# Performance work log

Hardware: AMD Instinct MI355X
Metric: run time of the kernel (lower is better)

Reference implementation:

```python
import jax, jax.numpy as jnp
import numpy as np

N_USERS = 100000
N_ITEMS = 100000
D = 64
B = 2048


def _ancf_layer(q, keys, aW, ab, W1, W2):
    # AttentionMechanism: hidden = relu(keys @ aW.T + ab)  [N, d]
    hidden = jax.nn.relu(keys @ aW.T + ab)
    # scores [B, N]; softmax over keys (dim=1)
    attn = jax.nn.softmax(q @ hidden.T, axis=1)
    q2 = q + attn @ keys  # [B, d]
    # MessageAggregation loop collapsed algebraically:
    # out = W1(q2) + sum_j W1(k_j) + sum_j W2(q2 * k_j)
    #     = W1(q2) + W1(S) + W2(q2 * S),  S = sum_j k_j
    S = keys.sum(axis=0)  # [d]
    out = (q2 + S) @ W1.T + (q2 * S) @ W2.T
    return jax.nn.leaky_relu(out, 0.01)


def setup_inputs() -> dict:
    key = jax.random.key(0)
    ks = jax.random.split(key, 12)
    scale_emb = 0.1
    scale_w = (2.0 / (D + D)) ** 0.5  # xavier-normal std for square layers
    inp = {
        "user_emb": jax.random.normal(ks[0], (N_USERS, D), jnp.float32) * scale_emb,
        "item_emb": jax.random.normal(ks[1], (N_ITEMS, D), jnp.float32) * scale_emb,
        "u_attn_W": jax.random.normal(ks[2], (D, D), jnp.float32) * scale_w,
        "u_attn_b": jnp.zeros((D,), jnp.float32),
        "u_W1": jax.random.normal(ks[3], (D, D), jnp.float32) * scale_w,
        "u_W2": jax.random.normal(ks[4], (D, D), jnp.float32) * scale_w,
        "i_attn_W": jax.random.normal(ks[5], (D, D), jnp.float32) * scale_w,
        "i_attn_b": jnp.zeros((D,), jnp.float32),
        "i_W1": jax.random.normal(ks[6], (D, D), jnp.float32) * scale_w,
        "i_W2": jax.random.normal(ks[7], (D, D), jnp.float32) * scale_w,
        "user_id": jax.random.randint(ks[8], (B,), 0, N_USERS),
        "item_id": jax.random.randint(ks[9], (B,), 0, N_ITEMS),
        "all_user_ids": jnp.arange(N_USERS),
        "all_item_ids": jnp.arange(N_ITEMS),
    }
    return inp


def reference(user_emb, item_emb, u_attn_W, u_attn_b, u_W1, u_W2,
              i_attn_W, i_attn_b, i_W1, i_W2,
              user_id, item_id, all_user_ids, all_item_ids):
    all_user_embeddings = user_emb[all_user_ids]  # [N_users, d]
    all_item_embeddings = item_emb[all_item_ids]  # [N_items, d]
    ue = all_user_embeddings[user_id]  # [B, d]
    ie = all_item_embeddings[item_id]  # [B, d]

    ue_out = _ancf_layer(ue, all_item_embeddings, u_attn_W, u_attn_b, u_W1, u_W2)
    ie_out = _ancf_layer(ie, all_user_embeddings, i_attn_W, i_attn_b, i_W1, i_W2)

    og_user = jnp.concatenate([ue, ue_out], axis=1)  # [B, 2d]
    og_item = jnp.concatenate([ie, ie_out], axis=1)  # [B, 2d]
    return og_user.T @ og_item  # [2d, 2d]
```

## Files before the change

### kernel.cpp

```cpp
#include <hip/hip_runtime.h>


typedef __bf16 bf16x8 __attribute__((ext_vector_type(8)));
typedef float f32x2 __attribute__((ext_vector_type(2)));
typedef float f32x4 __attribute__((ext_vector_type(4)));
typedef float f32x16 __attribute__((ext_vector_type(16)));
typedef unsigned int u32x4 __attribute__((ext_vector_type(4)));
typedef int i32x4 __attribute__((ext_vector_type(4)));
typedef int i32x8 __attribute__((ext_vector_type(8)));

static constexpr int NKEYS  = 100000;
static constexpr int NP     = 102400;
static constexpr int DIM    = 64;
static constexpr int BQ     = 2048;
static constexpr int NCH    = 64;
static constexpr int CHROWS = NP / NCH;
static constexpr int NPH    = CHROWS / 64;
static constexpr int NTIL   = NP / 64;
static constexpr float PADCNT = float(NP - NKEYS);
static constexpr float LOG2E  = 1.44269504088896340736f;

#define DEVINL __device__ __forceinline__

DEVINL unsigned int cvtpk(float lo, float hi) {
    unsigned int r;
    asm("v_cvt_pk_bf16_f32 %0, %1, %2" : "=v"(r) : "v"(lo), "v"(hi));
    return r;
}
DEVINL unsigned short bfr(float f) {
    return (unsigned short)(cvtpk(f, f) & 0xffffu);
}
DEVINL float bf2f(unsigned short u) {
    unsigned int w = (unsigned int)u << 16;
    return __builtin_bit_cast(float, w);
}
DEVINL void permswap(unsigned int& a, unsigned int& b) {
    asm("v_permlane32_swap_b32 %0, %1" : "+v"(a), "+v"(b));
}
DEVINL bf16x8 pack_frag(unsigned int w0, unsigned int w1, unsigned int w2, unsigned int w3) {
    u32x4 t; t[0] = w0; t[1] = w1; t[2] = w2; t[3] = w3;
    return __builtin_bit_cast(bf16x8, t);
}
DEVINL bf16x8 frag8_f32(const float* p) {
    f32x4 a = *reinterpret_cast<const f32x4*>(p);
    f32x4 b = *reinterpret_cast<const f32x4*>(p + 4);
    return pack_frag(cvtpk(a[0], a[1]), cvtpk(a[2], a[3]),
                     cvtpk(b[0], b[1]), cvtpk(b[2], b[3]));
}
DEVINL unsigned int fp8x4(float a, float b, float c, float d) {
    int r = __builtin_amdgcn_cvt_pk_fp8_f32(a, b, 0, false);
    r = __builtin_amdgcn_cvt_pk_fp8_f32(c, d, r, true);
    return (unsigned int)r;
}
DEVINL unsigned char fp8b(float f) {
    return (unsigned char)(__builtin_amdgcn_cvt_pk_fp8_f32(f, f, 0, false) & 0xFF);
}
DEVINL i32x8 cat8(i32x4 a, i32x4 b) {
    return __builtin_shufflevector(a, b, 0, 1, 2, 3, 4, 5, 6, 7);
}
DEVINL f32x16 mfma8(i32x8 a, i32x8 b, f32x16 c) {
    return __builtin_amdgcn_mfma_scale_f32_32x32x64_f8f6f4(
        a, b, c, 0 , 0 ,
        0, 0x7F7F7F7F, 0, 0x7F7F7F7F);
}
DEVINL float fexp2(float x) {
    float f = __builtin_fmaf(x, 8388608.0f, 1065713994.0f);
    int i = (int)f;
    return __builtin_bit_cast(float, i);
}
DEVINL f32x2 pkadd(f32x2 a, f32x2 b) {
    f32x2 r;
    asm("v_pk_add_f32 %0, %1, %2" : "=v"(r) : "v"(a), "v"(b));
    return r;
}

__global__ __launch_bounds__(256) void prep_kernel(
    const float* __restrict__ user_emb, const float* __restrict__ item_emb,
    const float* __restrict__ uaW, const float* __restrict__ uab,
    const float* __restrict__ iaW, const float* __restrict__ iab,
    unsigned char* __restrict__ Khid, unsigned char* __restrict__ Vpan,
    float* __restrict__ csum)
{
    const int side = blockIdx.y;
    const int tile = blockIdx.x;
    const float* keys = (side == 0) ? item_emb : user_emb;
    const float* aW   = (side == 0) ? uaW : iaW;
    const float* ab   = (side == 0) ? uab : iab;
    unsigned char* Kh  = Khid + (size_t)side * NP * DIM;
    unsigned char* Vps = Vpan + (size_t)side * (NP / 32) * 2048;

    __shared__ float Kf[64][68];
    __shared__ float Wf[64][68];
    __shared__ float bl[64];

    const int t  = threadIdx.x;
    const int r  = t >> 2;
    const int c0 = (t & 3) * 16;

    {
        const float4* src = reinterpret_cast<const float4*>(aW + r * 64 + c0);
        float4* dst = reinterpret_cast<float4*>(&Wf[r][c0]);
        #pragma unroll
        for (int q = 0; q < 4; ++q) dst[q] = src[q];
        if (t < 64) bl[t] = ab[t];
    }
    {
        const int n = tile * 64 + r;
        float4* dst = reinterpret_cast<float4*>(&Kf[r][c0]);
        if (n < NKEYS) {
            const float4* src = reinterpret_cast<const float4*>(keys + (size_t)n * 64 + c0);
            #pragma unroll
            for (int q = 0; q < 4; ++q) dst[q] = src[q];
        } else {
            const float4 z = make_float4(0.f, 0.f, 0.f, 0.f);
            #pragma unroll
            for (int q = 0; q < 4; ++q) dst[q] = z;
        }
    }
    __syncthreads();

    {
        const int wv = t >> 6, lane = t & 63;
        const int c = lane & 31, hi = lane >> 5;
        const int n0 = (wv & 1) * 32, j0 = (wv >> 1) * 32;
        f32x16 acc{};
        #pragma unroll
        for (int ks = 0; ks < 4; ++ks) {
            bf16x8 af = frag8_f32(&Kf[n0 + c][ks * 16 + hi * 8]);
            bf16x8 bf_ = frag8_f32(&Wf[j0 + c][ks * 16 + hi * 8]);
            acc = __builtin_amdgcn_mfma_f32_32x32x16_bf16(af, bf_, acc, 0, 0, 0);
        }
        const float bj = bl[j0 + c];
        #pragma unroll
        for (int rr = 0; rr < 16; ++rr) {
            const int n  = n0 + (rr & 3) + 8 * (rr >> 2) + 4 * hi;
            const int gn = tile * 64 + n;
            float h = fmaxf(acc[rr] + bj, 0.f);
            if (gn >= NKEYS) h = 0.f;
            Kh[(size_t)gn * 64 + j0 + c] = fp8b(h);
        }
    }
    {
        unsigned int pw[4];
        #pragma unroll
        for (int j = 0; j < 4; ++j)
            pw[j] = fp8x4(Kf[c0 + 4 * j][r],     Kf[c0 + 4 * j + 1][r],
                          Kf[c0 + 4 * j + 2][r], Kf[c0 + 4 * j + 3][r]);
        unsigned char* dst = Vps + ((size_t)(2 * tile + (c0 >> 5))) * 2048 + r * 32 + (c0 & 31);
        *reinterpret_cast<uint4*>(dst) = make_uint4(pw[0], pw[1], pw[2], pw[3]);
    }
    if (t < 64) {
        float s = 0.f;
        #pragma unroll 8
        for (int rr = 0; rr < 64; ++rr) s += Kf[rr][t];
        csum[((size_t)side * NTIL + tile) * 64 + t] = s;
    }
}

__global__ __launch_bounds__(64) void sreduceA_kernel(const float* __restrict__ csum,
                                                      float* __restrict__ csum2)
{
    const int j = blockIdx.x, side = blockIdx.y, d = threadIdx.x;
    float s = 0.f;
    for (int idx = j; idx < NTIL; idx += 64)
        s += csum[((size_t)side * NTIL + idx) * 64 + d];
    csum2[((size_t)side * 64 + j) * 64 + d] = s;
}

__global__ __launch_bounds__(64) void sreduceB_kernel(const float* __restrict__ csum2,
                                                      float* __restrict__ Sbuf)
{
    const int side = blockIdx.x, d = threadIdx.x;
    float s = 0.f;
    #pragma unroll 8
    for (int j = 0; j < 64; ++j) s += csum2[((size_t)side * 64 + j) * 64 + d];
    Sbuf[side * 64 + d] = s;
}

__global__ __launch_bounds__(512) void flash_kernel(
    const float* __restrict__ user_emb, const float* __restrict__ item_emb,
    const int* __restrict__ user_id, const int* __restrict__ item_id,
    const unsigned char* __restrict__ Khid, const unsigned char* __restrict__ Vpan,
    unsigned short* __restrict__ Opart, float* __restrict__ lpart)
{
    const int side  = blockIdx.z;
    const int chunk = blockIdx.x;
    const int qblk  = blockIdx.y;
    const int wave  = threadIdx.x >> 6;
    const int lane  = threadIdx.x & 63;
    const int c  = lane & 31;
    const int hi = lane >> 5;

    __shared__ __align__(16) unsigned char KV[2][8192];

    const float* emb = (side == 0) ? user_emb : item_emb;
    const int* ids   = (side == 0) ? user_id  : item_id;
    const unsigned char* Kh = Khid + ((size_t)side * NP + (size_t)chunk * CHROWS) * 64;
    const unsigned char* Vb = Vpan + ((size_t)side * (NP / 32) + (size_t)chunk * (CHROWS / 32)) * 2048;

    const unsigned char* gsrc;
    if (wave < 4) {
        const int st = wave >> 1, qh = wave & 1;
        gsrc = Kh + st * 2048 + qh * 16 + c * 64 + hi * 32;
    } else {
        const int dblk = (wave - 4) >> 1, qh = wave & 1;
        gsrc = Vb + dblk * 1024 + qh * 16 + hi * 2048 + c * 32;
    }

    const unsigned char* gnext = gsrc;
    int ibuf = 0;
    auto ISSUE = [&]() {
        __builtin_amdgcn_global_load_lds(
            (const __attribute__((address_space(1))) unsigned int*)gnext,
            (__attribute__((address_space(3))) unsigned int*)&KV[ibuf][wave * 1024],
            16, 0, 0);
        gnext += 4096;
        ibuf ^= 1;
    };

    const int qtile = qblk * 256 + wave * 32;
    const int id = ids[qtile + c];
    const float* qrow = emb + (size_t)id * 64 + hi * 32;
    float4 qf[8];
    #pragma unroll
    for (int w = 0; w < 8; ++w)
        qf[w] = *reinterpret_cast<const float4*>(qrow + w * 4);

    ISSUE();

    i32x8 bq;
    #pragma unroll
    for (int w = 0; w < 8; ++w)
        bq[w] = (int)fp8x4(qf[w].x * LOG2E, qf[w].y * LOG2E,
                           qf[w].z * LOG2E, qf[w].w * LOG2E);

    f32x16 o0{}, o1{};
    f32x2 lacc[8] = {};

    asm volatile("s_waitcnt vmcnt(0)" ::: "memory");
    __builtin_amdgcn_s_barrier();

    for (int p = 0; p < NPH; ++p) {
        if (p + 1 < NPH) ISSUE();

        const unsigned char* Bp = &KV[p & 1][0];
        const int fo = hi * 512 + c * 16;

        i32x8 ak0 = cat8(*reinterpret_cast<const i32x4*>(Bp + fo),
                         *reinterpret_cast<const i32x4*>(Bp + 1024 + fo));
        i32x8 ak1 = cat8(*reinterpret_cast<const i32x4*>(Bp + 2048 + fo),
                         *reinterpret_cast<const i32x4*>(Bp + 3072 + fo));

        __builtin_amdgcn_s_setprio(1);
        f32x16 z{};
        f32x16 s0 = mfma8(ak0, bq, z);
        f32x16 s1 = mfma8(ak1, bq, z);
        __builtin_amdgcn_s_setprio(0);

        i32x8 bv0 = cat8(*reinterpret_cast<const i32x4*>(Bp + 4096 + fo),
                         *reinterpret_cast<const i32x4*>(Bp + 5120 + fo));
        i32x8 bv1 = cat8(*reinterpret_cast<const i32x4*>(Bp + 6144 + fo),
                         *reinterpret_cast<const i32x4*>(Bp + 7168 + fo));

        #pragma unroll
        for (int rr = 0; rr < 16; ++rr) s0[rr] = fexp2(s0[rr]);
        #pragma unroll
        for (int rr = 0; rr < 16; ++rr) s1[rr] = fexp2(s1[rr]);

        #pragma unroll
        for (int g = 0; g < 8; ++g) {
            f32x2 a; a[0] = s0[2 * g]; a[1] = s0[2 * g + 1];
            f32x2 b; b[0] = s1[2 * g]; b[1] = s1[2 * g + 1];
            lacc[g] = pkadd(lacc[g], pkadd(a, b));
        }

        unsigned int p0[4], p1[4];
        #pragma unroll
        for (int g = 0; g < 4; ++g) {
            p0[g] = fp8x4(s0[4 * g], s0[4 * g + 1], s0[4 * g + 2], s0[4 * g + 3]);
            p1[g] = fp8x4(s1[4 * g], s1[4 * g + 1], s1[4 * g + 2], s1[4 * g + 3]);
            permswap(p0[g], p1[g]);
        }
        i32x8 pa;
        pa[0] = (int)p0[0]; pa[1] = (int)p1[0];
        pa[2] = (int)p0[1]; pa[3] = (int)p1[1];
        pa[4] = (int)p0[2]; pa[5] = (int)p1[2];
        pa[6] = (int)p0[3]; pa[7] = (int)p1[3];

        __builtin_amdgcn_s_setprio(1);
        o0 = mfma8(pa, bv0, o0);
        o1 = mfma8(pa, bv1, o1);
        __builtin_amdgcn_s_setprio(0);

        if (p + 1 < NPH) {
            asm volatile("s_waitcnt vmcnt(0)" ::: "memory");
            __builtin_amdgcn_s_barrier();
        }
    }

    float ls = 0.f;
    #pragma unroll
    for (int g = 0; g < 8; ++g) ls += lacc[g][0] + lacc[g][1];
    ls += __shfl_xor(ls, 32);

    unsigned short* Op = Opart + (((size_t)(side * NCH + chunk)) * BQ + qtile) * 64;
    #pragma unroll
    for (int rr = 0; rr < 16; ++rr) {
        const int q = (rr & 3) + 8 * (rr >> 2) + 4 * hi;
        Op[q * 64 + c]      = bfr(o0[rr]);
        Op[q * 64 + 32 + c] = bfr(o1[rr]);
    }
    if (hi == 0)
        lpart[((size_t)(side * NCH + chunk)) * BQ + qtile + c] = ls;
}

__global__ __launch_bounds__(64) void combine_kernel(
    const float* __restrict__ user_emb, const float* __restrict__ item_emb,
    const int* __restrict__ user_id, const int* __restrict__ item_id,
    const float* __restrict__ uW1, const float* __restrict__ uW2,
    const float* __restrict__ iW1, const float* __restrict__ iW2,
    const unsigned short* __restrict__ Opart, const float* __restrict__ lpart,
    const float* __restrict__ Sbuf,
    float* __restrict__ Aog, float* __restrict__ Bog)
{
    const int bid  = blockIdx.x;
    const int side = bid >> 11;
    const int q    = bid & (BQ - 1);
    const int d    = threadIdx.x;

    const unsigned short* Ob = Opart + ((size_t)side * NCH * BQ + q) * 64 + d;
    float num = 0.f;
    #pragma unroll 8
    for (int ch = 0; ch < NCH; ++ch)
        num += bf2f(Ob[(size_t)ch * BQ * 64]);
    const float* lb = lpart + (size_t)side * NCH * BQ + q;
    float lsum = -PADCNT * fexp2(0.0f);
    #pragma unroll 8
    for (int ch = 0; ch < NCH; ++ch)
        lsum += lb[(size_t)ch * BQ];

    const int id = ((side == 0) ? user_id : item_id)[q];
    const float* emb = (side == 0) ? user_emb : item_emb;
    const float e  = emb[(size_t)id * 64 + d];
    const float q2 = e + num / lsum;
    const float Sd = Sbuf[side * 64 + d];

    __shared__ float a1[64], a2[64];
    a1[d] = q2 + Sd;
    a2[d] = q2 * Sd;
    __syncthreads();

    const float* W1 = (side == 0) ? uW1 : iW1;
    const float* W2 = (side == 0) ? uW2 : iW2;
    float acc = 0.f;
    #pragma unroll 8
    for (int dd = 0; dd < 64; ++dd)
        acc += a1[dd] * W1[d * 64 + dd] + a2[dd] * W2[d * 64 + dd];
    const float out = (acc >= 0.f) ? acc : 0.01f * acc;

    float* og = (side == 0) ? Aog : Bog;
    og[(size_t)q * 128 + d]      = e;
    og[(size_t)q * 128 + 64 + d] = out;
}

__global__ __launch_bounds__(256) void final1_kernel(
    const float* __restrict__ Aog, const float* __restrict__ Bog, float* __restrict__ part)
{
    const int b = blockIdx.x;
    const int t = threadIdx.x;
    __shared__ float As[64][128];
    __shared__ float Bs[64][128];
    {
        float* Asf = &As[0][0];
        float* Bsf = &Bs[0][0];
        const float* Ab = Aog + (size_t)b * 64 * 128;
        const float* Bb = Bog + (size_t)b * 64 * 128;
        #pragma unroll
        for (int qq = 0; qq < 8; ++qq) {
            const int off = qq * 1024 + t * 4;
            *reinterpret_cast<float4*>(Asf + off) = *reinterpret_cast<const float4*>(Ab + off);
            *reinterpret_cast<float4*>(Bsf + off) = *reinterpret_cast<const float4*>(Bb + off);
        }
    }
    __syncthreads();

    const int i0 = (t >> 4) * 8, j0 = (t & 15) * 8;
    float acc[8][8] = {};
    for (int k = 0; k < 64; ++k) {
        float av[8], bv[8];
        *reinterpret_cast<f32x4*>(&av[0]) = *reinterpret_cast<const f32x4*>(&As[k][i0]);
        *reinterpret_cast<f32x4*>(&av[4]) = *reinterpret_cast<const f32x4*>(&As[k][i0 + 4]);
        *reinterpret_cast<f32x4*>(&bv[0]) = *reinterpret_cast<const f32x4*>(&Bs[k][j0]);
        *reinterpret_cast<f32x4*>(&bv[4]) = *reinterpret_cast<const f32x4*>(&Bs[k][j0 + 4]);
        #pragma unroll
        for (int ii = 0; ii < 8; ++ii)
            #pragma unroll
            for (int jj = 0; jj < 8; ++jj)
                acc[ii][jj] += av[ii] * bv[jj];
    }
    float* P = part + (size_t)b * 128 * 128;
    #pragma unroll
    for (int ii = 0; ii < 8; ++ii) {
        *reinterpret_cast<float4*>(P + (i0 + ii) * 128 + j0)     = *reinterpret_cast<float4*>(&acc[ii][0]);
        *reinterpret_cast<float4*>(P + (i0 + ii) * 128 + j0 + 4) = *reinterpret_cast<float4*>(&acc[ii][4]);
    }
}

__global__ __launch_bounds__(128) void final2_kernel(const float* __restrict__ part,
                                                     float* __restrict__ out)
{
    const int i = blockIdx.x, j = threadIdx.x;
    float s = 0.f;
    #pragma unroll 8
    for (int b = 0; b < 32; ++b) s += part[(size_t)b * 128 * 128 + i * 128 + j];
    out[i * 128 + j] = s;
}

extern "C" void kernel_launch(void* const* d_in, const int* in_sizes, int n_in,
                              void* d_out, int out_size, void* d_ws, size_t ws_size,
                              hipStream_t stream)
{
    (void)in_sizes; (void)n_in; (void)out_size; (void)ws_size;
    const float* user_emb = (const float*)d_in[0];
    const float* item_emb = (const float*)d_in[1];
    const float* uaW = (const float*)d_in[2];
    const float* uab = (const float*)d_in[3];
    const float* uW1 = (const float*)d_in[4];
    const float* uW2 = (const float*)d_in[5];
    const float* iaW = (const float*)d_in[6];
    const float* iab = (const float*)d_in[7];
    const float* iW1 = (const float*)d_in[8];
    const float* iW2 = (const float*)d_in[9];
    const int* user_id = (const int*)d_in[10];
    const int* item_id = (const int*)d_in[11];

    char* ws = (char*)d_ws;
    size_t off = 0;
    auto alloc = [&](size_t bytes) -> void* {
        void* p = ws + off;
        off = (off + bytes + 255) & ~(size_t)255;
        return p;
    };
    unsigned char* Khid8 = (unsigned char*)alloc((size_t)2 * NP * DIM);
    unsigned char* Vpan8 = (unsigned char*)alloc((size_t)2 * (NP / 32) * 2048);
    float* csum  = (float*)alloc((size_t)2 * NTIL * 64 * 4);
    float* csum2 = (float*)alloc((size_t)2 * 64 * 64 * 4);
    float* Sbuf  = (float*)alloc((size_t)2 * 64 * 4);
    unsigned short* Opart = (unsigned short*)alloc((size_t)2 * NCH * BQ * 64 * 2);
    float* lpart = (float*)alloc((size_t)2 * NCH * BQ * 4);
    float* Aog   = (float*)alloc((size_t)BQ * 128 * 4);
    float* Bog   = (float*)alloc((size_t)BQ * 128 * 4);
    float* Fpart = (float*)alloc((size_t)32 * 128 * 128 * 4);

    prep_kernel<<<dim3(NTIL, 2), 256, 0, stream>>>(user_emb, item_emb, uaW, uab, iaW, iab,
                                                   Khid8, Vpan8, csum);
    sreduceA_kernel<<<dim3(64, 2), 64, 0, stream>>>(csum, csum2);
    sreduceB_kernel<<<2, 64, 0, stream>>>(csum2, Sbuf);
    flash_kernel<<<dim3(NCH, BQ / 256, 2), 512, 0, stream>>>(user_emb, item_emb, user_id, item_id,
                                                             Khid8, Vpan8, Opart, lpart);
    combine_kernel<<<2 * BQ, 64, 0, stream>>>(user_emb, item_emb, user_id, item_id,
                                              uW1, uW2, iW1, iW2, Opart, lpart, Sbuf, Aog, Bog);
    final1_kernel<<<32, 256, 0, stream>>>(Aog, Bog, Fpart);
    final2_kernel<<<128, 128, 0, stream>>>(Fpart, (float*)d_out);
}
```

Baseline: 147.3 us.

## Transpose partial buffers and weights for coalesced combine; widen final reduction

Flash partial outputs and softmax denominators are now stored query-major so the combine step reads contiguous per-query chunk data, and lsum is reduced with wave shuffles. Combine packs four queries per block and reads pretransposed W1/W2 produced by a new small kernel, giving coalesced weight loads. The final outer-product is split across 128 blocks instead of 32, at the cost of a larger partial buffer and a longer final sum. Flash stores become more scattered in exchange.

```diff
diff --git a/kernel.cpp b/kernel.cpp
--- a/kernel.cpp
+++ b/kernel.cpp
@@ -177,6 +177,22 @@
     Sbuf[side * 64 + d] = s;
 }
 
+__global__ __launch_bounds__(256) void wtrans_kernel(
+    const float* __restrict__ uW1, const float* __restrict__ uW2,
+    const float* __restrict__ iW1, const float* __restrict__ iW2,
+    float* __restrict__ WT)
+{
+    const float* W = (blockIdx.x == 0) ? uW1 : (blockIdx.x == 1) ? uW2
+                   : (blockIdx.x == 2) ? iW1 : iW2;
+    float* T = WT + (size_t)blockIdx.x * 4096;
+    const int t = threadIdx.x;
+    const int j = t >> 2;
+    const int dd0 = (t & 3) * 16;
+    #pragma unroll
+    for (int k = 0; k < 16; ++k)
+        T[(dd0 + k) * 64 + j] = W[j * 64 + dd0 + k];
+}
+
 __global__ __launch_bounds__(512) void flash_kernel(
     const float* __restrict__ user_emb, const float* __restrict__ item_emb,
     const int* __restrict__ user_id, const int* __restrict__ item_id,
@@ -303,64 +319,64 @@
     for (int g = 0; g < 8; ++g) ls += lacc[g][0] + lacc[g][1];
     ls += __shfl_xor(ls, 32);
 
-    unsigned short* Op = Opart + (((size_t)(side * NCH + chunk)) * BQ + qtile) * 64;
+    unsigned short* Op = Opart + (((size_t)(side * BQ + qtile)) * NCH + chunk) * 64;
     #pragma unroll
     for (int rr = 0; rr < 16; ++rr) {
         const int q = (rr & 3) + 8 * (rr >> 2) + 4 * hi;
-        Op[q * 64 + c]      = bfr(o0[rr]);
-        Op[q * 64 + 32 + c] = bfr(o1[rr]);
+        Op[(size_t)q * NCH * 64 + c]      = bfr(o0[rr]);
+        Op[(size_t)q * NCH * 64 + 32 + c] = bfr(o1[rr]);
     }
     if (hi == 0)
-        lpart[((size_t)(side * NCH + chunk)) * BQ + qtile + c] = ls;
-}
-
-__global__ __launch_bounds__(64) void combine_kernel(
+        lpart[((size_t)(side * BQ + qtile + c)) * NCH + chunk] = ls;
+}
+
+__global__ __launch_bounds__(256) void combine_kernel(
     const float* __restrict__ user_emb, const float* __restrict__ item_emb,
     const int* __restrict__ user_id, const int* __restrict__ item_id,
-    const float* __restrict__ uW1, const float* __restrict__ uW2,
-    const float* __restrict__ iW1, const float* __restrict__ iW2,
+    const float* __restrict__ WT,
     const unsigned short* __restrict__ Opart, const float* __restrict__ lpart,
     const float* __restrict__ Sbuf,
     float* __restrict__ Aog, float* __restrict__ Bog)
 {
     const int bid  = blockIdx.x;
-    const int side = bid >> 11;
-    const int q    = bid & (BQ - 1);
-    const int d    = threadIdx.x;
-
-    const unsigned short* Ob = Opart + ((size_t)side * NCH * BQ + q) * 64 + d;
+    const int side = bid >> 9;
+    const int wave = threadIdx.x >> 6;
+    const int lane = threadIdx.x & 63;
+    const int q    = ((bid & 511) << 2) + wave;
+    const int j    = lane;
+
+    const unsigned short* Ob = Opart + ((size_t)(side * BQ + q)) * (NCH * 64) + j;
     float num = 0.f;
     #pragma unroll 8
     for (int ch = 0; ch < NCH; ++ch)
-        num += bf2f(Ob[(size_t)ch * BQ * 64]);
-    const float* lb = lpart + (size_t)side * NCH * BQ + q;
-    float lsum = -PADCNT * fexp2(0.0f);
-    #pragma unroll 8
-    for (int ch = 0; ch < NCH; ++ch)
-        lsum += lb[(size_t)ch * BQ];
+        num += bf2f(Ob[ch * 64]);
+
+    float lv = lpart[((size_t)(side * BQ + q)) * NCH + lane];
+    #pragma unroll
+    for (int m = 32; m >= 1; m >>= 1) lv += __shfl_xor(lv, m);
+    const float lsum = lv - PADCNT * fexp2(0.0f);
 
     const int id = ((side == 0) ? user_id : item_id)[q];
     const float* emb = (side == 0) ? user_emb : item_emb;
-    const float e  = emb[(size_t)id * 64 + d];
+    const float e  = emb[(size_t)id * 64 + j];
     const float q2 = e + num / lsum;
-    const float Sd = Sbuf[side * 64 + d];
-
-    __shared__ float a1[64], a2[64];
-    a1[d] = q2 + Sd;
-    a2[d] = q2 * Sd;
-    __syncthreads();
-
-    const float* W1 = (side == 0) ? uW1 : iW1;
-    const float* W2 = (side == 0) ? uW2 : iW2;
+    const float Sd = Sbuf[side * 64 + j];
+
+    __shared__ float a1s[4][64], a2s[4][64];
+    a1s[wave][j] = q2 + Sd;
+    a2s[wave][j] = q2 * Sd;
+
+    const float* W1T = WT + (size_t)side * 8192;
+    const float* W2T = W1T + 4096;
     float acc = 0.f;
     #pragma unroll 8
     for (int dd = 0; dd < 64; ++dd)
-        acc += a1[dd] * W1[d * 64 + dd] + a2[dd] * W2[d * 64 + dd];
+        acc += a1s[wave][dd] * W1T[dd * 64 + j] + a2s[wave][dd] * W2T[dd * 64 + j];
     const float out = (acc >= 0.f) ? acc : 0.01f * acc;
 
     float* og = (side == 0) ? Aog : Bog;
-    og[(size_t)q * 128 + d]      = e;
-    og[(size_t)q * 128 + 64 + d] = out;
+    og[(size_t)q * 128 + j]      = e;
+    og[(size_t)q * 128 + 64 + j] = out;
 }
 
 __global__ __launch_bounds__(256) void final1_kernel(
@@ -368,15 +384,15 @@
 {
     const int b = blockIdx.x;
     const int t = threadIdx.x;
-    __shared__ float As[64][128];
-    __shared__ float Bs[64][128];
+    __shared__ float As[16][128];
+    __shared__ float Bs[16][128];
     {
         float* Asf = &As[0][0];
         float* Bsf = &Bs[0][0];
-        const float* Ab = Aog + (size_t)b * 64 * 128;
-        const float* Bb = Bog + (size_t)b * 64 * 128;
-        #pragma unroll
-        for (int qq = 0; qq < 8; ++qq) {
+        const float* Ab = Aog + (size_t)b * 16 * 128;
+        const float* Bb = Bog + (size_t)b * 16 * 128;
+        #pragma unroll
+        for (int qq = 0; qq < 2; ++qq) {
             const int off = qq * 1024 + t * 4;
             *reinterpret_cast<float4*>(Asf + off) = *reinterpret_cast<const float4*>(Ab + off);
             *reinterpret_cast<float4*>(Bsf + off) = *reinterpret_cast<const float4*>(Bb + off);
@@ -386,7 +402,8 @@
 
     const int i0 = (t >> 4) * 8, j0 = (t & 15) * 8;
     float acc[8][8] = {};
-    for (int k = 0; k < 64; ++k) {
+    #pragma unroll
+    for (int k = 0; k < 16; ++k) {
         float av[8], bv[8];
         *reinterpret_cast<f32x4*>(&av[0]) = *reinterpret_cast<const f32x4*>(&As[k][i0]);
         *reinterpret_cast<f32x4*>(&av[4]) = *reinterpret_cast<const f32x4*>(&As[k][i0 + 4]);
@@ -412,7 +429,7 @@
     const int i = blockIdx.x, j = threadIdx.x;
     float s = 0.f;
     #pragma unroll 8
-    for (int b = 0; b < 32; ++b) s += part[(size_t)b * 128 * 128 + i * 128 + j];
+    for (int b = 0; b < 128; ++b) s += part[(size_t)b * 128 * 128 + i * 128 + j];
     out[i * 128 + j] = s;
 }
 
@@ -446,20 +463,22 @@
     float* csum  = (float*)alloc((size_t)2 * NTIL * 64 * 4);
     float* csum2 = (float*)alloc((size_t)2 * 64 * 64 * 4);
     float* Sbuf  = (float*)alloc((size_t)2 * 64 * 4);
-    unsigned short* Opart = (unsigned short*)alloc((size_t)2 * NCH * BQ * 64 * 2);
-    float* lpart = (float*)alloc((size_t)2 * NCH * BQ * 4);
+    float* WT    = (float*)alloc((size_t)4 * 4096 * 4);
+    unsigned short* Opart = (unsigned short*)alloc((size_t)2 * BQ * NCH * 64 * 2);
+    float* lpart = (float*)alloc((size_t)2 * BQ * NCH * 4);
     float* Aog   = (float*)alloc((size_t)BQ * 128 * 4);
     float* Bog   = (float*)alloc((size_t)BQ * 128 * 4);
-    float* Fpart = (float*)alloc((size_t)32 * 128 * 128 * 4);
+    float* Fpart = (float*)alloc((size_t)128 * 128 * 128 * 4);
 
     prep_kernel<<<dim3(NTIL, 2), 256, 0, stream>>>(user_emb, item_emb, uaW, uab, iaW, iab,
                                                    Khid8, Vpan8, csum);
     sreduceA_kernel<<<dim3(64, 2), 64, 0, stream>>>(csum, csum2);
     sreduceB_kernel<<<2, 64, 0, stream>>>(csum2, Sbuf);
+    wtrans_kernel<<<4, 256, 0, stream>>>(uW1, uW2, iW1, iW2, WT);
     flash_kernel<<<dim3(NCH, BQ / 256, 2), 512, 0, stream>>>(user_emb, item_emb, user_id, item_id,
                                                              Khid8, Vpan8, Opart, lpart);
-    combine_kernel<<<2 * BQ, 64, 0, stream>>>(user_emb, item_emb, user_id, item_id,
-                                              uW1, uW2, iW1, iW2, Opart, lpart, Sbuf, Aog, Bog);
-    final1_kernel<<<32, 256, 0, stream>>>(Aog, Bog, Fpart);
+    combine_kernel<<<2 * BQ / 4, 256, 0, stream>>>(user_emb, item_emb, user_id, item_id,
+                                                   WT, Opart, lpart, Sbuf, Aog, Bog);
+    final1_kernel<<<128, 256, 0, stream>>>(Aog, Bog, Fpart);
     final2_kernel<<<128, 128, 0, stream>>>(Fpart, (float*)d_out);
 }
```

Result: faster. 133.4 us (-9.4%).
